# Optimization experiments

Hardware: AMD Instinct MI355X
Metric: run time of the kernel (lower is better)

The kernel has to match this reference:

```python
import jax, jax.numpy as jnp
import numpy as np

D_STATE = 16
D_CONV = 4
DT_RANK = 16  # ceil(d_model/16) = ceil(256/16)
N_LAYERS = 2
EPS = 1e-5


def _layernorm(x, g, b):
    m = jnp.mean(x, -1, keepdims=True)
    v = jnp.var(x, -1, keepdims=True)
    return (x - m) * jax.lax.rsqrt(v + EPS) * g + b


def _causal_conv(x, w, b):
    # x [B,L,D], depthwise causal conv, w [D,K], b [D]
    K = w.shape[1]
    L = x.shape[1]
    xp = jnp.pad(x, ((0, 0), (K - 1, 0), (0, 0)))
    y = sum(xp[:, k:k + L, :] * w[:, k] for k in range(K))
    return y + b


def _selective_scan(u, dt, A, Bm, Cm, D_skip):
    # u, dt [B,L,d]; A [d,n]; Bm, Cm [B,L,n]; D_skip [d]
    def step(h, inp):
        dt_t, B_t, C_t, u_t = inp  # [B,d],[B,n],[B,n],[B,d]
        dA = jnp.exp(dt_t[:, :, None] * A)                      # [B,d,n]
        h = dA * h + dt_t[:, :, None] * B_t[:, None, :] * u_t[:, :, None]
        y = jnp.einsum('bdn,bn->bd', h, C_t)
        return h, y

    Bsz, L, d = u.shape
    h0 = jnp.zeros((Bsz, d, A.shape[1]), u.dtype)
    xs = (dt.transpose(1, 0, 2), Bm.transpose(1, 0, 2),
          Cm.transpose(1, 0, 2), u.transpose(1, 0, 2))
    _, ys = jax.lax.scan(step, h0, xs)                          # [L,B,d]
    return ys.transpose(1, 0, 2) + u * D_skip


def _mamba_block(x, Wip, cw, cb, Wxp, Wdt, bdt, Alog, Dp, Wout):
    xz = x @ Wip                                                # [B,L,2*d_inner]
    d_inner = Wip.shape[1] // 2
    xc, z = xz[..., :d_inner], xz[..., d_inner:]
    xc = jax.nn.silu(_causal_conv(xc, cw, cb))
    xdbl = xc @ Wxp                                             # [B,L,dt_rank+2n]
    dt = jax.nn.softplus(xdbl[..., :DT_RANK] @ Wdt + bdt)
    Bm = xdbl[..., DT_RANK:DT_RANK + D_STATE]
    Cm = xdbl[..., DT_RANK + D_STATE:]
    A = -jnp.exp(Alog)
    y = _selective_scan(xc, dt, A, Bm, Cm, Dp)
    y = y * jax.nn.silu(z)
    return y @ Wout


def reference(z_t, W_in, b_in, ln_g, ln_b, W_inproj, conv_w, conv_b, W_xproj,
              W_dt, b_dt, A_log, D_skip, W_out, W_outp, b_outp, lno_g, lno_b):
    x = z_t @ W_in + b_in                                       # [B,L,d_model]
    for i in range(N_LAYERS):
        res = x
        xn = _layernorm(x, ln_g[i], ln_b[i])
        x = res + _mamba_block(xn, W_inproj[i], conv_w[i], conv_b[i],
                               W_xproj[i], W_dt[i], b_dt[i], A_log[i],
                               D_skip[i], W_out[i])  # dropout is identity in eval
    u = x @ W_outp + b_outp
    return _layernorm(u, lno_g, lno_b)


def setup_inputs() -> dict:
    key = jax.random.key(0)
    B, L = 16, 2048
    d_input, d_model, d_output, d_inner = 1088, 256, 64, 512
    n = N_LAYERS
    ks = jax.random.split(key, 10)

    def rn(k, shape, fan):
        return jax.random.normal(k, shape, jnp.float32) / np.float32(np.sqrt(fan))

    A_init = jnp.log(jnp.arange(1, D_STATE + 1, dtype=jnp.float32))
    return {
        'z_t': jax.random.normal(ks[0], (B, L, d_input), jnp.float32),
        'W_in': rn(ks[1], (d_input, d_model), d_input),
        'b_in': jnp.zeros((d_model,), jnp.float32),
        'ln_g': jnp.ones((n, d_model), jnp.float32),
        'ln_b': jnp.zeros((n, d_model), jnp.float32),
        'W_inproj': rn(ks[2], (n, d_model, 2 * d_inner), d_model),
        'conv_w': rn(ks[3], (n, d_inner, D_CONV), D_CONV),
        'conv_b': jnp.zeros((n, d_inner), jnp.float32),
        'W_xproj': rn(ks[4], (n, d_inner, DT_RANK + 2 * D_STATE), d_inner),
        'W_dt': rn(ks[5], (n, DT_RANK, d_inner), DT_RANK),
        'b_dt': jnp.full((n, d_inner), -4.6, jnp.float32),  # softplus ~ 0.01
        'A_log': jnp.broadcast_to(A_init, (n, d_inner, D_STATE)) + 0.0,
        'D_skip': jnp.ones((n, d_inner), jnp.float32),
        'W_out': rn(ks[6], (n, d_inner, d_model), d_inner),
        'W_outp': rn(ks[7], (d_model, d_output), d_model),
        'b_outp': jnp.zeros((d_output,), jnp.float32),
        'lno_g': jnp.ones((d_output,), jnp.float32),
        'lno_b': jnp.zeros((d_output,), jnp.float32),
    }
```

## Files before the change

### kernel.cpp

```cpp
#include <hip/hip_runtime.h>
#include <hip/hip_bf16.h>
#include <math.h>
#include <stdint.h>

#define L_SEQ 2048
#define BATCH 16
#define NROWS (BATCH * L_SEQ)
#define DMODEL 256
#define DINNER 512
#define C_CH 32
#define T_CH 64
#define LOG2E 1.4426950408889634f

typedef __attribute__((ext_vector_type(8))) __bf16 bf16x8;
typedef __attribute__((ext_vector_type(4))) float f32x4;
typedef __attribute__((ext_vector_type(8))) unsigned short u16x8;
typedef __attribute__((address_space(1))) const uint32_t gu32;
typedef __attribute__((address_space(3))) uint32_t lu32;

#if __has_builtin(__builtin_amdgcn_exp2f)
#define EXP2F __builtin_amdgcn_exp2f
#else
#define EXP2F exp2f
#endif

__device__ __forceinline__ float sigmoidf_(float x) { return 1.f / (1.f + __expf(-x)); }

__device__ __forceinline__ unsigned short f2bf(float f) {
    union { float f; uint32_t u; } v; v.f = f;
    uint32_t r = v.u + 0x7FFF + ((v.u >> 16) & 1);
    return (unsigned short)(r >> 16);
}
__device__ __forceinline__ float bf2f(unsigned short h) {
    union { uint32_t u; float f; } v; v.u = ((uint32_t)h) << 16;
    return v.f;
}

__device__ __forceinline__ void gld16(const void* g, void* l) {
    __builtin_amdgcn_global_load_lds((gu32*)g, (lu32*)l, 16, 0, 0);
}

__global__ __launch_bounds__(256) void wtrans(const float* __restrict__ W,
                                              unsigned short* __restrict__ Wt, int K, int N) {
    int idx = blockIdx.x * 256 + threadIdx.x;
    if (idx < K * N) {
        int n = idx / K, k = idx % K;
        Wt[idx] = f2bf(W[(size_t)k * N + n]);
    }
}
__global__ __launch_bounds__(256) void wtrans_pad(const float* __restrict__ W,
                                                  unsigned short* __restrict__ Wt,
                                                  int K, int Nreal, int Npad) {
    int idx = blockIdx.x * 256 + threadIdx.x;
    if (idx < Npad * K) {
        int n = idx / K, k = idx % K;
        Wt[idx] = (n < Nreal) ? f2bf(W[(size_t)k * Nreal + n]) : (unsigned short)0;
    }
}

template <int TM, bool A_F32, bool HAS_BIAS, bool HAS_RES, bool OUT_BF16>
__global__ __launch_bounds__(256) void gemm_bf16(
    const void* __restrict__ Aptr, const unsigned short* __restrict__ Bt,
    const float* __restrict__ bias, const float* __restrict__ res,
    void* __restrict__ Cout, int M, int N, int K, int Nout)
{
    constexpr int MR = TM / 32;
    constexpr int ABYTES = TM * 32 * (A_F32 ? 4 : 2);
    __shared__ __align__(16) char AldsRaw[2][ABYTES];
    __shared__ unsigned short Blds[2][4096];
    const int tid = threadIdx.x;
    const int w = tid >> 6, lane = tid & 63;

    const int nwg = gridDim.x;
    const int q = nwg >> 3;
    const int wg = (blockIdx.x & 7) * q + (blockIdx.x >> 3);
    const int nx = N >> 7;
    const int bm = (wg / nx) * TM, bn = (wg % nx) * 128;

    const int wr = (w >> 1) * (TM / 2), wc = (w & 1) * 64;
    const int fr = lane & 15, fq = lane >> 4;
    const size_t KbB = (size_t)K * 2;
    const size_t KbA = (size_t)K * (A_F32 ? 4 : 2);

    const int o0 = tid * 16, o1 = (256 + tid) * 16;
    const int ar0 = o0 >> 6, ac0 = o0 & 63;
    const int ar1 = o1 >> 6, ac1 = o1 & 63;
    const int arow = tid >> 3;
    const int acolb = (o0 & 127) ^ ((arow & 7) << 4);

    const char* Ab = (const char*)Aptr;
    const char* Bb = (const char*)Bt;
    const int lds0 = w * 1024, lds1 = 4096 + w * 1024;

    f32x4 acc[MR][4];
#pragma unroll
    for (int m = 0; m < MR; m++)
#pragma unroll
        for (int n = 0; n < 4; n++) acc[m][n] = (f32x4){0.f, 0.f, 0.f, 0.f};

    auto stageB = [&](int buf, int k0) {
        char* lB = (char*)Blds[buf];
        gld16(Bb + (size_t)(bn + ar0) * KbB + (k0 << 1) + ac0, lB + lds0);
        gld16(Bb + (size_t)(bn + ar1) * KbB + (k0 << 1) + ac1, lB + lds1);
    };
    auto stageA = [&](int buf, int k0) {
        char* lA = AldsRaw[buf];
        if constexpr (A_F32) {
#pragma unroll
            for (int i = 0; i < TM / 32; i++)
                gld16(Ab + (size_t)(bm + i * 32 + arow) * KbA + ((size_t)k0 * 4) + acolb,
                      lA + i * 4096 + lds0);
        } else {
            gld16(Ab + (size_t)(bm + ar0) * KbA + (k0 << 1) + ac0, lA + lds0);
            if constexpr (TM == 128)
                gld16(Ab + (size_t)(bm + ar1) * KbA + (k0 << 1) + ac1, lA + lds1);
        }
    };
    auto compute = [&](int buf) {
        bf16x8 af[MR], bg[4];
        if constexpr (A_F32) {
            const char* lA = AldsRaw[buf];
#pragma unroll
            for (int m = 0; m < MR; m++) {
                const int row = wr + m * 16 + fr;
                const int sw = (row & 7) << 4;
                const int b0 = row * 128 + fq * 32;
                float4 x0 = *(const float4*)(lA + (b0 ^ sw));
                float4 x1 = *(const float4*)(lA + ((b0 + 16) ^ sw));
                bf16x8 a;
                a[0]=(__bf16)x0.x; a[1]=(__bf16)x0.y; a[2]=(__bf16)x0.z; a[3]=(__bf16)x0.w;
                a[4]=(__bf16)x1.x; a[5]=(__bf16)x1.y; a[6]=(__bf16)x1.z; a[7]=(__bf16)x1.w;
                af[m] = a;
            }
        } else {
            const unsigned short* lA = (const unsigned short*)AldsRaw[buf];
#pragma unroll
            for (int m = 0; m < MR; m++)
                af[m] = *(const bf16x8*)&lA[(wr + m * 16 + fr) * 32 + fq * 8];
        }
#pragma unroll
        for (int n = 0; n < 4; n++)
            bg[n] = *(const bf16x8*)&Blds[buf][(wc + n * 16 + fr) * 32 + fq * 8];
#pragma unroll
        for (int m = 0; m < MR; m++)
#pragma unroll
            for (int n = 0; n < 4; n++)
                acc[m][n] = __builtin_amdgcn_mfma_f32_16x16x32_bf16(af[m], bg[n], acc[m][n], 0, 0, 0);
    };

    stageA(0, 0); stageB(0, 0);
    asm volatile("s_waitcnt vmcnt(0) lgkmcnt(0)" ::: "memory");
    __builtin_amdgcn_s_barrier();
    __builtin_amdgcn_sched_barrier(0);

    constexpr int VOPS = (A_F32 ? (TM / 32) : (TM == 128 ? 2 : 1)) + 2;
    const int NT = K >> 5;
    for (int kt = 0; kt < NT; ++kt) {
        const int cur = kt & 1;
        const bool has_next = (kt + 1 < NT);
        if (has_next) {
            const int k0 = (kt + 1) << 5;
            stageA(cur ^ 1, k0); stageB(cur ^ 1, k0);
        }
        if (has_next) {
            if constexpr (VOPS == 6)      asm volatile("s_waitcnt vmcnt(6)" ::: "memory");
            else if constexpr (VOPS == 4) asm volatile("s_waitcnt vmcnt(4)" ::: "memory");
            else                          asm volatile("s_waitcnt vmcnt(3)" ::: "memory");
        } else {
            asm volatile("s_waitcnt vmcnt(0)" ::: "memory");
        }
        __builtin_amdgcn_s_barrier();
        __builtin_amdgcn_sched_barrier(0);

        compute(cur);

        asm volatile("s_waitcnt lgkmcnt(0)" ::: "memory");
        __builtin_amdgcn_s_barrier();
        __builtin_amdgcn_sched_barrier(0);
    }

#pragma unroll
    for (int m = 0; m < MR; m++) {
#pragma unroll
        for (int n = 0; n < 4; n++) {
            int col = bn + wc + n * 16 + fr;
            if (col < Nout) {
#pragma unroll
                for (int r = 0; r < 4; r++) {
                    int row = bm + wr + m * 16 + fq * 4 + r;
                    float v = acc[m][n][r];
                    if (HAS_BIAS) v += bias[col];
                    if (HAS_RES)  v += res[(size_t)row * Nout + col];
                    if (OUT_BF16) ((unsigned short*)Cout)[(size_t)row * Nout + col] = f2bf(v);
                    else          ((float*)Cout)[(size_t)row * Nout + col] = v;
                }
            }
        }
    }
}

__global__ __launch_bounds__(256) void ln256(
    const float* __restrict__ x, const float* __restrict__ g,
    const float* __restrict__ b, unsigned short* __restrict__ out)
{
    int lane = threadIdx.x & 63, wid = threadIdx.x >> 6;
    size_t r = (size_t)blockIdx.x * 4 + wid;
    const float4 v = *(const float4*)&x[r * 256 + lane * 4];
    float s = v.x + v.y + v.z + v.w;
    float sq = v.x * v.x + v.y * v.y + v.z * v.z + v.w * v.w;
#pragma unroll
    for (int off = 32; off; off >>= 1) { s += __shfl_xor(s, off); sq += __shfl_xor(sq, off); }
    float mean = s * (1.f / 256.f);
    float var = sq * (1.f / 256.f) - mean * mean;
    float rs = rsqrtf(var + 1e-5f);
    float4 gv = *(const float4*)&g[lane * 4];
    float4 bv = *(const float4*)&b[lane * 4];
    ushort4 o;
    o.x = f2bf((v.x - mean) * rs * gv.x + bv.x);
    o.y = f2bf((v.y - mean) * rs * gv.y + bv.y);
    o.z = f2bf((v.z - mean) * rs * gv.z + bv.z);
    o.w = f2bf((v.w - mean) * rs * gv.w + bv.w);
    *(ushort4*)&out[r * 256 + lane * 4] = o;
}

__global__ __launch_bounds__(256) void ln64(
    const float* __restrict__ t, const float* __restrict__ g,
    const float* __restrict__ b, float* __restrict__ out)
{
    int lane = threadIdx.x & 63, wid = threadIdx.x >> 6;
    size_t r = (size_t)blockIdx.x * 4 + wid;
    float v = t[r * 64 + lane];
    float s = v, sq = v * v;
#pragma unroll
    for (int off = 32; off; off >>= 1) { s += __shfl_xor(s, off); sq += __shfl_xor(sq, off); }
    float mean = s * (1.f / 64.f);
    float var = sq * (1.f / 64.f) - mean * mean;
    out[r * 64 + lane] = (v - mean) * rsqrtf(var + 1e-5f) * g[lane] + b[lane];
}

__global__ __launch_bounds__(256) void conv_silu8(
    const unsigned short* __restrict__ xz, const float* __restrict__ w,
    const float* __restrict__ cb, unsigned short* __restrict__ xc)
{
    int idx = blockIdx.x * 256 + threadIdx.x;
    int d8 = (idx & 63) << 3;
    int l  = (idx >> 6) & 2047;
    int b  = idx >> 17;
    const unsigned short* base = xz + ((size_t)b * L_SEQ + l) * 1024 + d8;
    u16x8 t0 = {0,0,0,0,0,0,0,0}, t1 = t0, t2 = t0;
    u16x8 t3 = *(const u16x8*)base;
    if (l >= 1) t2 = *(const u16x8*)(base - 1024);
    if (l >= 2) t1 = *(const u16x8*)(base - 2048);
    if (l >= 3) t0 = *(const u16x8*)(base - 3072);
    u16x8 o;
#pragma unroll
    for (int j = 0; j < 8; j++) {
        float4 wv = *(const float4*)&w[(d8 + j) * 4];
        float acc = cb[d8 + j];
        acc = fmaf(bf2f(t0[j]), wv.x, acc);
        acc = fmaf(bf2f(t1[j]), wv.y, acc);
        acc = fmaf(bf2f(t2[j]), wv.z, acc);
        acc = fmaf(bf2f(t3[j]), wv.w, acc);
        o[j] = f2bf(acc * sigmoidf_(acc));
    }
    *(u16x8*)&xc[((size_t)b * L_SEQ + l) * 512 + d8] = o;
}

__global__ __launch_bounds__(256) void scan_pass1(
    const unsigned short* __restrict__ xc, const float* __restrict__ xdbl,
    const float* __restrict__ Wdt, const float* __restrict__ bdt,
    const float* __restrict__ Alog,
    float* __restrict__ Pbuf, float* __restrict__ Sbuf)
{
    __shared__ float xs[T_CH][32];
    int idx = blockIdx.x * 256 + threadIdx.x;
    int d = idx & 511;
    int c = (idx >> 9) & (C_CH - 1);
    int b = idx >> 14;
    size_t r0 = (size_t)b * L_SEQ + (size_t)c * T_CH;
#pragma unroll
    for (int ii = 0; ii < 2; ii++) {
        int i = threadIdx.x + ii * 256, row = i >> 3, qq = i & 7;
        *(float4*)&xs[row][qq * 4] = *(const float4*)&xdbl[(r0 + row) * 48 + qq * 4];
    }
    __syncthreads();

    float wdt[16];
#pragma unroll
    for (int j = 0; j < 16; j++) wdt[j] = Wdt[j * 512 + d];
    const float bd = bdt[d];

    float a[16], a2[16], S[16];
#pragma unroll
    for (int n = 0; n < 16; n++) a[n] = -__expf(Alog[d * 16 + n]);
#pragma unroll
    for (int n = 0; n < 16; n++) a2[n] = a[n] * LOG2E;
#pragma unroll
    for (int n = 0; n < 16; n++) S[n] = 0.f;
    bool pow_ok = true;
#pragma unroll
    for (int n = 1; n < 16; n++)
        pow_ok = pow_ok && (fabsf(a[n] - (n + 1) * a[0]) <= 1e-3f * (n + 1) * fabsf(a[0]));
    const float a0l2 = a[0] * LOG2E;
    float Tsum = 0.f;

    if (pow_ok) {
        for (int t = 0; t < T_CH; t++) {
            float dtr = bd;
#pragma unroll
            for (int j = 0; j < 16; j++) dtr = fmaf(xs[t][j], wdt[j], dtr);
            float dtv = (dtr > 20.f) ? dtr : __logf(1.f + __expf(dtr));
            float u = bf2f(xc[(r0 + t) * 512 + d]);
            float dtu = dtv * u;
            Tsum += dtv;
            float e1 = EXP2F(dtv * a0l2), e2 = e1 * e1;
            S[0] = fmaf(e1, S[0], dtu * xs[t][16]);
            S[1] = fmaf(e2, S[1], dtu * xs[t][17]);
            float pm2 = e1, pm1 = e2;
#pragma unroll
            for (int n = 2; n < 16; n++) {
                float cur = pm2 * e2;
                S[n] = fmaf(cur, S[n], dtu * xs[t][16 + n]);
                pm2 = pm1; pm1 = cur;
            }
        }
    } else {
        for (int t = 0; t < T_CH; t++) {
            float dtr = bd;
#pragma unroll
            for (int j = 0; j < 16; j++) dtr = fmaf(xs[t][j], wdt[j], dtr);
            float dtv = (dtr > 20.f) ? dtr : __logf(1.f + __expf(dtr));
            float u = bf2f(xc[(r0 + t) * 512 + d]);
            float dtu = dtv * u;
            Tsum += dtv;
#pragma unroll
            for (int n = 0; n < 16; n++) {
                float dA = EXP2F(dtv * a2[n]);
                S[n] = fmaf(dA, S[n], dtu * xs[t][16 + n]);
            }
        }
    }
    size_t o = (size_t)idx * 16;
#pragma unroll
    for (int qq = 0; qq < 4; qq++) {
        float4 pv = make_float4(EXP2F(Tsum * a2[qq*4]),   EXP2F(Tsum * a2[qq*4+1]),
                                EXP2F(Tsum * a2[qq*4+2]), EXP2F(Tsum * a2[qq*4+3]));
        *(float4*)&Pbuf[o + qq * 4] = pv;
        *(float4*)&Sbuf[o + qq * 4] = make_float4(S[qq*4], S[qq*4+1], S[qq*4+2], S[qq*4+3]);
    }
}

__global__ __launch_bounds__(256) void scan_pass2(
    const float* __restrict__ Pbuf, float* __restrict__ Sbuf)
{
    int g = blockIdx.x * 256 + threadIdx.x;
    int nd = g & 8191;
    int b = g >> 13;
    float H = 0.f;
    for (int c = 0; c < C_CH; c++) {
        size_t idx = ((size_t)(b * C_CH + c) * 8192) + nd;
        float P = Pbuf[idx], S = Sbuf[idx];
        float Hn = fmaf(P, H, S);
        Sbuf[idx] = H;
        H = Hn;
    }
}

__global__ __launch_bounds__(256) void scan_pass3(
    const unsigned short* __restrict__ xcin, const unsigned short* __restrict__ xz,
    const float* __restrict__ xdbl, const float* __restrict__ Wdt,
    const float* __restrict__ bdt, const float* __restrict__ Alog,
    const float* __restrict__ Dsk, const float* __restrict__ Sbuf,
    unsigned short* __restrict__ y)
{
    __shared__ float xs[T_CH][48];
    int idx = blockIdx.x * 256 + threadIdx.x;
    int d = idx & 511;
    int c = (idx >> 9) & (C_CH - 1);
    int b = idx >> 14;
    size_t r0 = (size_t)b * L_SEQ + (size_t)c * T_CH;
#pragma unroll
    for (int ii = 0; ii < 3; ii++) {
        int i = threadIdx.x + ii * 256, row = i / 12, qq = i % 12;
        *(float4*)&xs[row][qq * 4] = *(const float4*)&xdbl[(r0 + row) * 48 + qq * 4];
    }
    __syncthreads();

    float wdt[16];
#pragma unroll
    for (int j = 0; j < 16; j++) wdt[j] = Wdt[j * 512 + d];
    const float bd = bdt[d];

    float a[16], a2[16], h[16];
#pragma unroll
    for (int n = 0; n < 16; n++) a[n] = -__expf(Alog[d * 16 + n]);
#pragma unroll
    for (int n = 0; n < 16; n++) a2[n] = a[n] * LOG2E;
    {
        size_t o = (size_t)idx * 16;
#pragma unroll
        for (int qq = 0; qq < 4; qq++) {
            float4 v = *(const float4*)&Sbuf[o + qq * 4];
            h[qq*4] = v.x; h[qq*4+1] = v.y; h[qq*4+2] = v.z; h[qq*4+3] = v.w;
        }
    }
    bool pow_ok = true;
#pragma unroll
    for (int n = 1; n < 16; n++)
        pow_ok = pow_ok && (fabsf(a[n] - (n + 1) * a[0]) <= 1e-3f * (n + 1) * fabsf(a[0]));
    const float a0l2 = a[0] * LOG2E;
    const float Dv = Dsk[d];

    if (pow_ok) {
        for (int t = 0; t < T_CH; t++) {
            size_t ridx = (r0 + t) * 512 + d;
            float dtr = bd;
#pragma unroll
            for (int j = 0; j < 16; j++) dtr = fmaf(xs[t][j], wdt[j], dtr);
            float dtv = (dtr > 20.f) ? dtr : __logf(1.f + __expf(dtr));
            float u = bf2f(xcin[ridx]);
            float dtu = dtv * u;
            float e1 = EXP2F(dtv * a0l2), e2 = e1 * e1;
            float yv = 0.f;
            h[0] = fmaf(e1, h[0], dtu * xs[t][16]);  yv = fmaf(h[0], xs[t][32], yv);
            h[1] = fmaf(e2, h[1], dtu * xs[t][17]);  yv = fmaf(h[1], xs[t][33], yv);
            float pm2 = e1, pm1 = e2;
#pragma unroll
            for (int n = 2; n < 16; n++) {
                float cur = pm2 * e2;
                h[n] = fmaf(cur, h[n], dtu * xs[t][16 + n]);
                yv = fmaf(h[n], xs[t][32 + n], yv);
                pm2 = pm1; pm1 = cur;
            }
            yv = fmaf(u, Dv, yv);
            float z = bf2f(xz[(r0 + t) * 1024 + 512 + d]);
            y[ridx] = f2bf(yv * z * sigmoidf_(z));
        }
    } else {
        for (int t = 0; t < T_CH; t++) {
            size_t ridx = (r0 + t) * 512 + d;
            float dtr = bd;
#pragma unroll
            for (int j = 0; j < 16; j++) dtr = fmaf(xs[t][j], wdt[j], dtr);
            float dtv = (dtr > 20.f) ? dtr : __logf(1.f + __expf(dtr));
            float u = bf2f(xcin[ridx]);
            float dtu = dtv * u;
            float yv = 0.f;
#pragma unroll
            for (int n = 0; n < 16; n++) {
                float dA = EXP2F(dtv * a2[n]);
                h[n] = fmaf(dA, h[n], dtu * xs[t][16 + n]);
                yv = fmaf(h[n], xs[t][32 + n], yv);
            }
            yv = fmaf(u, Dv, yv);
            float z = bf2f(xz[(r0 + t) * 1024 + 512 + d]);
            y[ridx] = f2bf(yv * z * sigmoidf_(z));
        }
    }
}

extern "C" void kernel_launch(void* const* d_in, const int* in_sizes, int n_in,
                              void* d_out, int out_size, void* d_ws, size_t ws_size,
                              hipStream_t stream)
{
    const float* z_t     = (const float*)d_in[0];
    const float* W_in    = (const float*)d_in[1];
    const float* b_in    = (const float*)d_in[2];
    const float* ln_g    = (const float*)d_in[3];
    const float* ln_b    = (const float*)d_in[4];
    const float* W_inpr  = (const float*)d_in[5];
    const float* conv_w  = (const float*)d_in[6];
    const float* conv_b  = (const float*)d_in[7];
    const float* W_xproj = (const float*)d_in[8];
    const float* W_dt    = (const float*)d_in[9];
    const float* b_dt    = (const float*)d_in[10];
    const float* A_log   = (const float*)d_in[11];
    const float* D_skip  = (const float*)d_in[12];
    const float* W_out   = (const float*)d_in[13];
    const float* W_outp  = (const float*)d_in[14];
    const float* b_outp  = (const float*)d_in[15];
    const float* lno_g   = (const float*)d_in[16];
    const float* lno_b   = (const float*)d_in[17];
    float* out           = (float*)d_out;

    char* p = (char*)d_ws;
    float*          x    = (float*)p;          p += (size_t)NROWS * DMODEL * 4;
    unsigned short* xn   = (unsigned short*)p; p += (size_t)NROWS * DMODEL * 2;
    unsigned short* xc   = (unsigned short*)p; p += (size_t)NROWS * DINNER * 2;
    unsigned short* xz   = (unsigned short*)p; p += (size_t)NROWS * 1024 * 2;
    float*          xdbl = (float*)p;          p += (size_t)NROWS * 48 * 4;
    float*          Pbuf = (float*)p;          p += (size_t)BATCH * C_CH * DINNER * 16 * 4;
    float*          Sbuf = (float*)p;          p += (size_t)BATCH * C_CH * DINNER * 16 * 4;
    unsigned short* WinT  = (unsigned short*)p; p += (size_t)256 * 1088 * 2;
    unsigned short* WipT  = (unsigned short*)p; p += (size_t)2 * 1024 * 256 * 2;
    unsigned short* WoutT = (unsigned short*)p; p += (size_t)2 * 256 * 512 * 2;
    unsigned short* WxpT  = (unsigned short*)p; p += (size_t)2 * 128 * 512 * 2;
    unsigned short* WopT  = (unsigned short*)p; p += (size_t)128 * 256 * 2;
    float*          otmp = Pbuf;

    wtrans<<<(256 * 1088 + 255) / 256, 256, 0, stream>>>(W_in, WinT, 1088, 256);
    for (int l = 0; l < 2; l++) {
        wtrans<<<(1024 * 256 + 255) / 256, 256, 0, stream>>>(
            W_inpr + (size_t)l * 256 * 1024, WipT + (size_t)l * 1024 * 256, 256, 1024);
        wtrans<<<(256 * 512 + 255) / 256, 256, 0, stream>>>(
            W_out + (size_t)l * 512 * 256, WoutT + (size_t)l * 256 * 512, 512, 256);
        wtrans_pad<<<(128 * 512 + 255) / 256, 256, 0, stream>>>(
            W_xproj + (size_t)l * 512 * 48, WxpT + (size_t)l * 128 * 512, 512, 48, 128);
    }
    wtrans_pad<<<(128 * 256 + 255) / 256, 256, 0, stream>>>(W_outp, WopT, 256, 64, 128);

    gemm_bf16<64, true, true, false, false><<<(NROWS / 64) * (256 / 128), 256, 0, stream>>>(
        z_t, WinT, b_in, nullptr, x, NROWS, 256, 1088, 256);

    for (int layer = 0; layer < 2; ++layer) {
        ln256<<<NROWS / 4, 256, 0, stream>>>(x, ln_g + layer * 256, ln_b + layer * 256, xn);
        gemm_bf16<128, false, false, false, true><<<(NROWS / 128) * (1024 / 128), 256, 0, stream>>>(
            xn, WipT + (size_t)layer * 1024 * 256, nullptr, nullptr, xz, NROWS, 1024, 256, 1024);
        conv_silu8<<<NROWS * 64 / 256, 256, 0, stream>>>(
            xz, conv_w + layer * 512 * 4, conv_b + layer * 512, xc);
        gemm_bf16<64, false, false, false, false><<<(NROWS / 64) * (128 / 128), 256, 0, stream>>>(
            xc, WxpT + (size_t)layer * 128 * 512, nullptr, nullptr, xdbl, NROWS, 128, 512, 48);

        const float* Al_l  = A_log + layer * 512 * 16;
        const float* Wdt_l = W_dt + layer * 16 * 512;
        const float* bdt_l = b_dt + layer * 512;
        scan_pass1<<<BATCH * C_CH * DINNER / 256, 256, 0, stream>>>(
            xc, xdbl, Wdt_l, bdt_l, Al_l, Pbuf, Sbuf);
        scan_pass2<<<BATCH * DINNER * 16 / 256, 256, 0, stream>>>(Pbuf, Sbuf);
        scan_pass3<<<BATCH * C_CH * DINNER / 256, 256, 0, stream>>>(
            xc, xz, xdbl, Wdt_l, bdt_l, Al_l, D_skip + layer * 512, Sbuf, xc);

        if (layer == 0) {
            gemm_bf16<64, false, false, true, false><<<(NROWS / 64) * (256 / 128), 256, 0, stream>>>(
                xc, WoutT, nullptr, x, x, NROWS, 256, 512, 256);
        } else {
            gemm_bf16<64, false, false, true, true><<<(NROWS / 64) * (256 / 128), 256, 0, stream>>>(
                xc, WoutT + (size_t)256 * 512, nullptr, x, xn, NROWS, 256, 512, 256);
        }
    }

    gemm_bf16<64, false, true, false, false><<<(NROWS / 64) * (128 / 128), 256, 0, stream>>>(
        xn, WopT, b_outp, nullptr, otmp, NROWS, 128, 256, 64);
    ln64<<<NROWS / 4, 256, 0, stream>>>(otmp, lno_g, lno_b, out);
}
```

Measured before the change: 571.7 us.

## Generalize GEMM K-tile with swizzled LDS; store chunk dt-sums instead of decay matrix

The GEMM kernel gains a BK template parameter and is written generically with XOR-swizzled LDS layout for rows of 128 bytes or more. Several GEMMs now use a 64-wide K tile, which halves the number of barrier-separated iterations and raises the number of MFMAs per sync, at the cost of more LDS and registers. Scan pass 1 now writes only the per-chunk dt sum per channel instead of a full 16-state decay array. Pass 2 recomputes the decay with exp2, which cuts a large intermediate write and read for a small amount of extra arithmetic.

```diff
diff --git a/kernel.cpp b/kernel.cpp
--- a/kernel.cpp
+++ b/kernel.cpp
@@ -40,6 +40,14 @@
     __builtin_amdgcn_global_load_lds((gu32*)g, (lu32*)l, 16, 0, 0);
 }
 
+template <int N> __device__ __forceinline__ void waitv() {
+    if constexpr (N == 0)      asm volatile("s_waitcnt vmcnt(0)" ::: "memory");
+    else if constexpr (N == 3) asm volatile("s_waitcnt vmcnt(3)" ::: "memory");
+    else if constexpr (N == 4) asm volatile("s_waitcnt vmcnt(4)" ::: "memory");
+    else if constexpr (N == 6) asm volatile("s_waitcnt vmcnt(6)" ::: "memory");
+    else if constexpr (N == 8) asm volatile("s_waitcnt vmcnt(8)" ::: "memory");
+}
+
 __global__ __launch_bounds__(256) void wtrans(const float* __restrict__ W,
                                               unsigned short* __restrict__ Wt, int K, int N) {
     int idx = blockIdx.x * 256 + threadIdx.x;
@@ -58,16 +66,26 @@
     }
 }
 
-template <int TM, bool A_F32, bool HAS_BIAS, bool HAS_RES, bool OUT_BF16>
+template <int TM, int BK, bool A_F32, bool HAS_BIAS, bool HAS_RES, bool OUT_BF16>
 __global__ __launch_bounds__(256) void gemm_bf16(
     const void* __restrict__ Aptr, const unsigned short* __restrict__ Bt,
     const float* __restrict__ bias, const float* __restrict__ res,
     void* __restrict__ Cout, int M, int N, int K, int Nout)
 {
     constexpr int MR = TM / 32;
-    constexpr int ABYTES = TM * 32 * (A_F32 ? 4 : 2);
-    __shared__ __align__(16) char AldsRaw[2][ABYTES];
-    __shared__ unsigned short Blds[2][4096];
+    constexpr int EWA = A_F32 ? 4 : 2;
+    constexpr int RBA = BK * EWA;
+    constexpr int RBB = BK * 2;
+    constexpr int ABYTES = TM * RBA;
+    constexpr int BBYTES = 128 * RBB;
+    constexpr int OPSA = ABYTES / 4096;
+    constexpr int OPSB = BBYTES / 4096;
+    constexpr int VOPS = OPSA + OPSB;
+    constexpr bool SWZA = (RBA >= 128);
+    constexpr bool SWZB = (RBB >= 128);
+    constexpr int KK = BK / 32;
+    __shared__ __align__(16) char Alds[2][ABYTES];
+    __shared__ __align__(16) char Blds[2][BBYTES];
     const int tid = threadIdx.x;
     const int w = tid >> 6, lane = tid & 63;
 
@@ -80,17 +98,11 @@
     const int wr = (w >> 1) * (TM / 2), wc = (w & 1) * 64;
     const int fr = lane & 15, fq = lane >> 4;
     const size_t KbB = (size_t)K * 2;
-    const size_t KbA = (size_t)K * (A_F32 ? 4 : 2);
-
-    const int o0 = tid * 16, o1 = (256 + tid) * 16;
-    const int ar0 = o0 >> 6, ac0 = o0 & 63;
-    const int ar1 = o1 >> 6, ac1 = o1 & 63;
-    const int arow = tid >> 3;
-    const int acolb = (o0 & 127) ^ ((arow & 7) << 4);
+    const size_t KbA = (size_t)K * EWA;
 
     const char* Ab = (const char*)Aptr;
     const char* Bb = (const char*)Bt;
-    const int lds0 = w * 1024, lds1 = 4096 + w * 1024;
+    const int lds0 = w * 1024;
 
     f32x4 acc[MR][4];
 #pragma unroll
@@ -98,76 +110,89 @@
 #pragma unroll
         for (int n = 0; n < 4; n++) acc[m][n] = (f32x4){0.f, 0.f, 0.f, 0.f};
 
+    auto stageA = [&](int buf, int k0) {
+        char* lA = Alds[buf];
+#pragma unroll
+        for (int i = 0; i < OPSA; i++) {
+            const int o = i * 4096 + tid * 16;
+            const int row = o / RBA;
+            int col = o % RBA;
+            if constexpr (SWZA) col ^= (row & 7) << 4;
+            gld16(Ab + (size_t)(bm + row) * KbA + (size_t)k0 * EWA + col,
+                  lA + i * 4096 + lds0);
+        }
+    };
     auto stageB = [&](int buf, int k0) {
-        char* lB = (char*)Blds[buf];
-        gld16(Bb + (size_t)(bn + ar0) * KbB + (k0 << 1) + ac0, lB + lds0);
-        gld16(Bb + (size_t)(bn + ar1) * KbB + (k0 << 1) + ac1, lB + lds1);
-    };
-    auto stageA = [&](int buf, int k0) {
-        char* lA = AldsRaw[buf];
-        if constexpr (A_F32) {
-#pragma unroll
-            for (int i = 0; i < TM / 32; i++)
-                gld16(Ab + (size_t)(bm + i * 32 + arow) * KbA + ((size_t)k0 * 4) + acolb,
-                      lA + i * 4096 + lds0);
-        } else {
-            gld16(Ab + (size_t)(bm + ar0) * KbA + (k0 << 1) + ac0, lA + lds0);
-            if constexpr (TM == 128)
-                gld16(Ab + (size_t)(bm + ar1) * KbA + (k0 << 1) + ac1, lA + lds1);
+        char* lB = Blds[buf];
+#pragma unroll
+        for (int i = 0; i < OPSB; i++) {
+            const int o = i * 4096 + tid * 16;
+            const int row = o / RBB;
+            int col = o % RBB;
+            if constexpr (SWZB) col ^= (row & 7) << 4;
+            gld16(Bb + (size_t)(bn + row) * KbB + (size_t)k0 * 2 + col,
+                  lB + i * 4096 + lds0);
         }
     };
     auto compute = [&](int buf) {
-        bf16x8 af[MR], bg[4];
-        if constexpr (A_F32) {
-            const char* lA = AldsRaw[buf];
-#pragma unroll
-            for (int m = 0; m < MR; m++) {
-                const int row = wr + m * 16 + fr;
-                const int sw = (row & 7) << 4;
-                const int b0 = row * 128 + fq * 32;
-                float4 x0 = *(const float4*)(lA + (b0 ^ sw));
-                float4 x1 = *(const float4*)(lA + ((b0 + 16) ^ sw));
-                bf16x8 a;
-                a[0]=(__bf16)x0.x; a[1]=(__bf16)x0.y; a[2]=(__bf16)x0.z; a[3]=(__bf16)x0.w;
-                a[4]=(__bf16)x1.x; a[5]=(__bf16)x1.y; a[6]=(__bf16)x1.z; a[7]=(__bf16)x1.w;
-                af[m] = a;
-            }
-        } else {
-            const unsigned short* lA = (const unsigned short*)AldsRaw[buf];
+        bf16x8 af[MR][KK], bg[4][KK];
+        const char* lA = Alds[buf];
+        const char* lB = Blds[buf];
+#pragma unroll
+        for (int m = 0; m < MR; m++) {
+            const int row = wr + m * 16 + fr;
+            const int sw = SWZA ? ((row & 7) << 4) : 0;
+#pragma unroll
+            for (int kk = 0; kk < KK; kk++) {
+                if constexpr (A_F32) {
+                    const int b0 = row * RBA + kk * 128 + fq * 32;
+                    float4 x0 = *(const float4*)(lA + (b0 ^ sw));
+                    float4 x1 = *(const float4*)(lA + ((b0 + 16) ^ sw));
+                    bf16x8 a;
+                    a[0]=(__bf16)x0.x; a[1]=(__bf16)x0.y; a[2]=(__bf16)x0.z; a[3]=(__bf16)x0.w;
+                    a[4]=(__bf16)x1.x; a[5]=(__bf16)x1.y; a[6]=(__bf16)x1.z; a[7]=(__bf16)x1.w;
+                    af[m][kk] = a;
+                } else {
+                    const int c = kk * 64 + fq * 16;
+                    af[m][kk] = *(const bf16x8*)(lA + row * RBA + (c ^ sw));
+                }
+            }
+        }
+#pragma unroll
+        for (int n = 0; n < 4; n++) {
+            const int row = wc + n * 16 + fr;
+            const int sw = SWZB ? ((row & 7) << 4) : 0;
+#pragma unroll
+            for (int kk = 0; kk < KK; kk++) {
+                const int c = kk * 64 + fq * 16;
+                bg[n][kk] = *(const bf16x8*)(lB + row * RBB + (c ^ sw));
+            }
+        }
+#pragma unroll
+        for (int kk = 0; kk < KK; kk++)
 #pragma unroll
             for (int m = 0; m < MR; m++)
-                af[m] = *(const bf16x8*)&lA[(wr + m * 16 + fr) * 32 + fq * 8];
-        }
-#pragma unroll
-        for (int n = 0; n < 4; n++)
-            bg[n] = *(const bf16x8*)&Blds[buf][(wc + n * 16 + fr) * 32 + fq * 8];
-#pragma unroll
-        for (int m = 0; m < MR; m++)
-#pragma unroll
-            for (int n = 0; n < 4; n++)
-                acc[m][n] = __builtin_amdgcn_mfma_f32_16x16x32_bf16(af[m], bg[n], acc[m][n], 0, 0, 0);
+#pragma unroll
+                for (int n = 0; n < 4; n++)
+                    acc[m][n] = __builtin_amdgcn_mfma_f32_16x16x32_bf16(af[m][kk], bg[n][kk], acc[m][n], 0, 0, 0);
     };
+
+    const int NT = K / BK;
 
     stageA(0, 0); stageB(0, 0);
     asm volatile("s_waitcnt vmcnt(0) lgkmcnt(0)" ::: "memory");
     __builtin_amdgcn_s_barrier();
     __builtin_amdgcn_sched_barrier(0);
 
-    constexpr int VOPS = (A_F32 ? (TM / 32) : (TM == 128 ? 2 : 1)) + 2;
-    const int NT = K >> 5;
     for (int kt = 0; kt < NT; ++kt) {
         const int cur = kt & 1;
         const bool has_next = (kt + 1 < NT);
         if (has_next) {
-            const int k0 = (kt + 1) << 5;
+            const int k0 = (kt + 1) * BK;
             stageA(cur ^ 1, k0); stageB(cur ^ 1, k0);
-        }
-        if (has_next) {
-            if constexpr (VOPS == 6)      asm volatile("s_waitcnt vmcnt(6)" ::: "memory");
-            else if constexpr (VOPS == 4) asm volatile("s_waitcnt vmcnt(4)" ::: "memory");
-            else                          asm volatile("s_waitcnt vmcnt(3)" ::: "memory");
+            waitv<VOPS>();
         } else {
-            asm volatile("s_waitcnt vmcnt(0)" ::: "memory");
+            waitv<0>();
         }
         __builtin_amdgcn_s_barrier();
         __builtin_amdgcn_sched_barrier(0);
@@ -270,7 +295,7 @@
     const unsigned short* __restrict__ xc, const float* __restrict__ xdbl,
     const float* __restrict__ Wdt, const float* __restrict__ bdt,
     const float* __restrict__ Alog,
-    float* __restrict__ Pbuf, float* __restrict__ Sbuf)
+    float* __restrict__ Tbuf, float* __restrict__ Sbuf)
 {
     __shared__ float xs[T_CH][32];
     int idx = blockIdx.x * 256 + threadIdx.x;
@@ -340,26 +365,29 @@
             }
         }
     }
+    Tbuf[idx] = Tsum;
     size_t o = (size_t)idx * 16;
 #pragma unroll
-    for (int qq = 0; qq < 4; qq++) {
-        float4 pv = make_float4(EXP2F(Tsum * a2[qq*4]),   EXP2F(Tsum * a2[qq*4+1]),
-                                EXP2F(Tsum * a2[qq*4+2]), EXP2F(Tsum * a2[qq*4+3]));
-        *(float4*)&Pbuf[o + qq * 4] = pv;
+    for (int qq = 0; qq < 4; qq++)
         *(float4*)&Sbuf[o + qq * 4] = make_float4(S[qq*4], S[qq*4+1], S[qq*4+2], S[qq*4+3]);
-    }
 }
 
 __global__ __launch_bounds__(256) void scan_pass2(
-    const float* __restrict__ Pbuf, float* __restrict__ Sbuf)
+    const float* __restrict__ Tbuf, const float* __restrict__ Alog,
+    float* __restrict__ Sbuf)
 {
     int g = blockIdx.x * 256 + threadIdx.x;
     int nd = g & 8191;
     int b = g >> 13;
+    int d = nd >> 4, n = nd & 15;
+    const float a2 = -__expf(Alog[d * 16 + n]) * LOG2E;
     float H = 0.f;
     for (int c = 0; c < C_CH; c++) {
-        size_t idx = ((size_t)(b * C_CH + c) * 8192) + nd;
-        float P = Pbuf[idx], S = Sbuf[idx];
+        size_t base = (size_t)(b * C_CH + c);
+        float T = Tbuf[base * 512 + d];
+        float P = EXP2F(T * a2);
+        size_t idx = base * 8192 + nd;
+        float S = Sbuf[idx];
         float Hn = fmaf(P, H, S);
         Sbuf[idx] = H;
         H = Hn;
@@ -489,14 +517,15 @@
     unsigned short* xc   = (unsigned short*)p; p += (size_t)NROWS * DINNER * 2;
     unsigned short* xz   = (unsigned short*)p; p += (size_t)NROWS * 1024 * 2;
     float*          xdbl = (float*)p;          p += (size_t)NROWS * 48 * 4;
-    float*          Pbuf = (float*)p;          p += (size_t)BATCH * C_CH * DINNER * 16 * 4;
+    float*          Pregion = (float*)p;       p += (size_t)BATCH * C_CH * DINNER * 16 * 4;
     float*          Sbuf = (float*)p;          p += (size_t)BATCH * C_CH * DINNER * 16 * 4;
     unsigned short* WinT  = (unsigned short*)p; p += (size_t)256 * 1088 * 2;
     unsigned short* WipT  = (unsigned short*)p; p += (size_t)2 * 1024 * 256 * 2;
     unsigned short* WoutT = (unsigned short*)p; p += (size_t)2 * 256 * 512 * 2;
     unsigned short* WxpT  = (unsigned short*)p; p += (size_t)2 * 128 * 512 * 2;
     unsigned short* WopT  = (unsigned short*)p; p += (size_t)128 * 256 * 2;
-    float*          otmp = Pbuf;
+    float* Tbuf = Pregion;
+    float* otmp = Pregion;
 
     wtrans<<<(256 * 1088 + 255) / 256, 256, 0, stream>>>(W_in, WinT, 1088, 256);
     for (int l = 0; l < 2; l++) {
@@ -509,37 +538,37 @@
     }
     wtrans_pad<<<(128 * 256 + 255) / 256, 256, 0, stream>>>(W_outp, WopT, 256, 64, 128);
 
-    gemm_bf16<64, true, true, false, false><<<(NROWS / 64) * (256 / 128), 256, 0, stream>>>(
+    gemm_bf16<64, 64, true, true, false, false><<<(NROWS / 64) * (256 / 128), 256, 0, stream>>>(
         z_t, WinT, b_in, nullptr, x, NROWS, 256, 1088, 256);
 
     for (int layer = 0; layer < 2; ++layer) {
         ln256<<<NROWS / 4, 256, 0, stream>>>(x, ln_g + layer * 256, ln_b + layer * 256, xn);
-        gemm_bf16<128, false, false, false, true><<<(NROWS / 128) * (1024 / 128), 256, 0, stream>>>(
+        gemm_bf16<128, 32, false, false, false, true><<<(NROWS / 128) * (1024 / 128), 256, 0, stream>>>(
             xn, WipT + (size_t)layer * 1024 * 256, nullptr, nullptr, xz, NROWS, 1024, 256, 1024);
         conv_silu8<<<NROWS * 64 / 256, 256, 0, stream>>>(
             xz, conv_w + layer * 512 * 4, conv_b + layer * 512, xc);
-        gemm_bf16<64, false, false, false, false><<<(NROWS / 64) * (128 / 128), 256, 0, stream>>>(
+        gemm_bf16<64, 64, false, false, false, false><<<(NROWS / 64) * (128 / 128), 256, 0, stream>>>(
             xc, WxpT + (size_t)layer * 128 * 512, nullptr, nullptr, xdbl, NROWS, 128, 512, 48);
 
         const float* Al_l  = A_log + layer * 512 * 16;
         const float* Wdt_l = W_dt + layer * 16 * 512;
         const float* bdt_l = b_dt + layer * 512;
         scan_pass1<<<BATCH * C_CH * DINNER / 256, 256, 0, stream>>>(
-            xc, xdbl, Wdt_l, bdt_l, Al_l, Pbuf, Sbuf);
-        scan_pass2<<<BATCH * DINNER * 16 / 256, 256, 0, stream>>>(Pbuf, Sbuf);
+            xc, xdbl, Wdt_l, bdt_l, Al_l, Tbuf, Sbuf);
+        scan_pass2<<<BATCH * DINNER * 16 / 256, 256, 0, stream>>>(Tbuf, Al_l, Sbuf);
         scan_pass3<<<BATCH * C_CH * DINNER / 256, 256, 0, stream>>>(
             xc, xz, xdbl, Wdt_l, bdt_l, Al_l, D_skip + layer * 512, Sbuf, xc);
 
         if (layer == 0) {
-            gemm_bf16<64, false, false, true, false><<<(NROWS / 64) * (256 / 128), 256, 0, stream>>>(
+            gemm_bf16<64, 64, false, false, true, false><<<(NROWS / 64) * (256 / 128), 256, 0, stream>>>(
                 xc, WoutT, nullptr, x, x, NROWS, 256, 512, 256);
         } else {
-            gemm_bf16<64, false, false, true, true><<<(NROWS / 64) * (256 / 128), 256, 0, stream>>>(
+            gemm_bf16<64, 64, false, false, true, true><<<(NROWS / 64) * (256 / 128), 256, 0, stream>>>(
                 xc, WoutT + (size_t)256 * 512, nullptr, x, xn, NROWS, 256, 512, 256);
         }
     }
 
-    gemm_bf16<64, false, true, false, false><<<(NROWS / 64) * (128 / 128), 256, 0, stream>>>(
+    gemm_bf16<64, 32, false, true, false, false><<<(NROWS / 64) * (128 / 128), 256, 0, stream>>>(
         xn, WopT, b_outp, nullptr, otmp, NROWS, 128, 256, 64);
     ln64<<<NROWS / 4, 256, 0, stream>>>(otmp, lno_g, lno_b, out);
 }
```

After: 549.2 us. 3.9% less time.
